# Kernel tuning notes

Hardware: AMD Instinct MI355X
Metric: run time of the kernel (lower is better)

Reference implementation:

```python
import jax, jax.numpy as jnp
import numpy as np

LAT = (4, 24, 24, 24, 24, 3, 3)  # [mu, L0, L1, L2, L3, 3, 3]


def setup_inputs() -> dict:
    key = jax.random.key(0)
    k1, k2 = jax.random.split(key)
    U_re = jax.random.normal(k1, LAT, dtype=jnp.float32)
    U_im = jax.random.normal(k2, LAT, dtype=jnp.float32)
    return {"U_re": U_re, "U_im": U_im}


def _polyakov_dir(Umu, axis, L):
    """P(x) = prod_{k=0}^{L-1} U_mu(x + k*mu_hat) via a sequential scan of
    batched 3x3 complex matmuls. Umu: [L0,L1,L2,L3,3,3] complex."""

    def step(carry, _):
        P, Ush = carry
        Ush = jnp.roll(Ush, -1, axis=axis)  # U_mu(x + (k)*mu_hat)
        P = jnp.einsum('...ij,...jk->...ik', P, Ush)
        return (P, Ush), None

    (P, _), _ = jax.lax.scan(step, (Umu, Umu), None, length=L - 1)
    return P


def reference(U_re, U_im):
    U = jax.lax.complex(U_re, U_im)  # complex64 link field
    loops = jnp.stack([
        _polyakov_dir(U[mu], mu, U.shape[1 + mu]) for mu in range(4)
    ])  # [4, L0, L1, L2, L3, 3, 3] complex
    # return real/imag stacked so output is a real array
    return jnp.stack([loops.real, loops.imag])
```

## Files before the change

kernel.cpp:

```cpp
#include <hip/hip_runtime.h>

#define LSIZE 24
#define VOL (LSIZE*LSIZE*LSIZE*LSIZE)
#define NLINES (LSIZE*LSIZE*LSIZE)
#define LPB 32
#define TPB 256
#define ESTRIDE 71
#define BUFW (18*ESTRIDE)

__device__ __forceinline__ void cmul(const float* __restrict__ ar, const float* __restrict__ ai,
                                     const float* __restrict__ br, const float* __restrict__ bi,
                                     float* __restrict__ or_, float* __restrict__ oi_) {
#pragma unroll
  for (int i = 0; i < 3; ++i) {
#pragma unroll
    for (int j = 0; j < 3; ++j) {
      float sr = 0.f, si = 0.f;
#pragma unroll
      for (int m = 0; m < 3; ++m) {
        float x = ar[i*3+m], y = ai[i*3+m];
        float u = br[m*3+j], v = bi[m*3+j];
        sr = fmaf(x, u, sr);
        sr = fmaf(-y, v, sr);
        si = fmaf(x, v, si);
        si = fmaf(y, u, si);
      }
      or_[i*3+j] = sr;
      oi_[i*3+j] = si;
    }
  }
}

__device__ __forceinline__ void cp9(float* dr, float* di, const float* sr, const float* si) {
#pragma unroll
  for (int e = 0; e < 9; ++e) { dr[e] = sr[e]; di[e] = si[e]; }
}

__device__ __forceinline__ void setid(float* r, float* im) {
#pragma unroll
  for (int e = 0; e < 9; ++e) { r[e] = (e == 0 || e == 4 || e == 8) ? 1.f : 0.f; im[e] = 0.f; }
}

__device__ __forceinline__ void shup(float* dr, float* di, const float* sr, const float* si, int delta) {
#pragma unroll
  for (int e = 0; e < 9; ++e) {
    dr[e] = __shfl_up(sr[e], (unsigned)delta, 64);
    di[e] = __shfl_up(si[e], (unsigned)delta, 64);
  }
}
__device__ __forceinline__ void shdn(float* dr, float* di, const float* sr, const float* si, int delta) {
#pragma unroll
  for (int e = 0; e < 9; ++e) {
    dr[e] = __shfl_down(sr[e], (unsigned)delta, 64);
    di[e] = __shfl_down(si[e], (unsigned)delta, 64);
  }
}

__global__ __launch_bounds__(TPB, 4) void polyakov_hyb(
    const float* __restrict__ U_re, const float* __restrict__ U_im,
    float* __restrict__ out) {
  __shared__ float buf[4 * BUFW];

  const int lane = threadIdx.x & 63;
  const int wv   = threadIdx.x >> 6;
  const int mu   = (blockIdx.x * LPB) / NLINES;

  int tl, ll, sh;
  if (mu == 3) { tl = lane & 7; ll = lane >> 3; sh = 1; }
  else         { tl = lane >> 3; ll = lane & 7; sh = 8; }

  const int l0 = blockIdx.x * LPB + wv * 8 - mu * NLINES;
  const int l  = l0 + ll;
  const int cC = l % LSIZE;
  const int cB = (l / LSIZE) % LSIZE;
  const int cA = l / (LSIZE*LSIZE);

  int x0, x1, x2, x3, st;
  if (mu == 0)      { x0 = 0;  x1 = cA; x2 = cB; x3 = cC; st = LSIZE*LSIZE*LSIZE; }
  else if (mu == 1) { x0 = cA; x1 = 0;  x2 = cB; x3 = cC; st = LSIZE*LSIZE; }
  else if (mu == 2) { x0 = cA; x1 = cB; x2 = 0;  x3 = cC; st = LSIZE; }
  else              { x0 = cA; x1 = cB; x2 = cC; x3 = 0;  st = 1; }
  const int s0 = ((x0*LSIZE + x1)*LSIZE + x2)*LSIZE + x3;
  const int k0 = 3 * tl;

  const float* __restrict__ gR = U_re + (size_t)mu * (VOL*9);
  const float* __restrict__ gI = U_im + (size_t)mu * (VOL*9);
  float* __restrict__ oR = out + (size_t)mu * (VOL*9);
  float* __restrict__ oI = out + (size_t)(4 + mu) * (VOL*9);

  auto ldU = [&](int kk, float* r, float* im_) {
    const float* p = gR + (size_t)(s0 + kk*st) * 9;
    const float* q = gI + (size_t)(s0 + kk*st) * 9;
#pragma unroll
    for (int e = 0; e < 9; ++e) { r[e] = p[e]; im_[e] = q[e]; }
  };

  float* wbuf = buf + wv * BUFW;

  auto emit = [&](const float* Vr, const float* Vi, int j) {
    if (mu == 3) {
      float* pr = oR + (size_t)(s0 + (k0 + j) * st) * 9;
      float* pi = oI + (size_t)(s0 + (k0 + j) * st) * 9;
#pragma unroll
      for (int e = 0; e < 9; ++e) { pr[e] = Vr[e]; pi[e] = Vi[e]; }
    } else {
      asm volatile("s_waitcnt lgkmcnt(0)" ::: "memory");
#pragma unroll
      for (int e = 0; e < 9; ++e) {
        wbuf[e * ESTRIDE + lane]       = Vr[e];
        wbuf[(9 + e) * ESTRIDE + lane] = Vi[e];
      }
      asm volatile("s_waitcnt lgkmcnt(0)" ::: "memory");
      __builtin_amdgcn_sched_barrier(0);
      const int s0w = s0 - ll;
      int slab = 0, rem = lane;
#pragma unroll
      for (int p = 0; p < 9; ++p) {
        int line8 = rem / 9;
        int e = rem - line8 * 9;
        int m = (slab << 3) + line8;
        float vr = wbuf[e * ESTRIDE + m];
        float vi = wbuf[(9 + e) * ESTRIDE + m];
        size_t off = (size_t)(s0w + (3 * slab + j) * st) * 9 + rem;
        oR[off] = vr;
        oI[off] = vi;
        int rem2 = rem + 64;
        int c = rem2 >= 72;
        rem = c ? rem2 - 72 : rem2;
        slab += c;
      }
    }
  };

  float Br[9], Bi[9];
  {
    float Ar[9], Ai[9], Cr[9], Ci[9], Tr0[9], Ti0[9];
    ldU(k0 + 0, Ar, Ai);
    ldU(k0 + 1, Cr, Ci);
    cmul(Ar, Ai, Cr, Ci, Tr0, Ti0);
    ldU(k0 + 2, Ar, Ai);
    cmul(Tr0, Ti0, Ar, Ai, Br, Bi);
  }

  float Yr[9], Yi[9], Tr[9], Ti[9];

  float Pr[9], Pi[9];
  {
    float Xr[9], Xi[9];
    cp9(Xr, Xi, Br, Bi);
#pragma unroll
    for (int d = 1; d < 8; d <<= 1) {
      shup(Yr, Yi, Xr, Xi, d * sh);
      if (tl >= d) { cmul(Yr, Yi, Xr, Xi, Tr, Ti); cp9(Xr, Xi, Tr, Ti); }
    }
    shup(Pr, Pi, Xr, Xi, sh);
    if (tl == 0) setid(Pr, Pi);
  }

  float Rr[9], Ri[9];
  {
    float Zr[9], Zi[9];
    cp9(Zr, Zi, Br, Bi);
#pragma unroll
    for (int d = 1; d < 8; d <<= 1) {
      shdn(Yr, Yi, Zr, Zi, d * sh);
      if (tl + d < 8) { cmul(Zr, Zi, Yr, Yi, Tr, Ti); cp9(Zr, Zi, Tr, Ti); }
    }
    shdn(Yr, Yi, Zr, Zi, sh);
    if (tl == 7) setid(Yr, Yi);
    cmul(Yr, Yi, Pr, Pi, Rr, Ri);
  }

  cmul(Br, Bi, Rr, Ri, Tr, Ti);
  emit(Tr, Ti, 0);

  float W2r[9], W2i[9], U1r[9], U1i[9];
  ldU(k0 + 2, Yr, Yi);
  cmul(Yr, Yi, Rr, Ri, W2r, W2i);
  ldU(k0 + 1, U1r, U1i);
  float W1r[9], W1i[9];
  cmul(U1r, U1i, W2r, W2i, W1r, W1i);
  ldU(k0 + 0, Pr, Pi);

  cmul(W1r, W1i, Pr, Pi, Tr, Ti);
  emit(Tr, Ti, 1);
  cmul(W2r, W2i, Pr, Pi, Yr, Yi);
  cmul(Yr, Yi, U1r, U1i, Tr, Ti);
  emit(Tr, Ti, 2);
}

extern "C" void kernel_launch(void* const* d_in, const int* in_sizes, int n_in,
                              void* d_out, int out_size, void* d_ws, size_t ws_size,
                              hipStream_t stream) {
  const float* U_re = (const float*)d_in[0];
  const float* U_im = (const float*)d_in[1];
  float* out = (float*)d_out;
  int nblocks = 4 * NLINES / LPB;
  hipLaunchKernelGGL(polyakov_hyb, dim3(nblocks), dim3(TPB), 0, stream, U_re, U_im, out);
}
```

Measured before the change: 212.6 us.

## Stage links through LDS with direct global-to-LDS loads and vectorized stores

```diff
diff --git a/kernel.cpp b/kernel.cpp
--- a/kernel.cpp
+++ b/kernel.cpp
@@ -3,10 +3,10 @@
 #define LSIZE 24
 #define VOL (LSIZE*LSIZE*LSIZE*LSIZE)
 #define NLINES (LSIZE*LSIZE*LSIZE)
-#define LPB 32
-#define TPB 256
-#define ESTRIDE 71
-#define BUFW (18*ESTRIDE)
+#define LPB 8
+#define TPB 64
+#define IMG 1728
+#define NCHUNK 864
 
 __device__ __forceinline__ void cmul(const float* __restrict__ ar, const float* __restrict__ ai,
                                      const float* __restrict__ br, const float* __restrict__ bi,
@@ -56,93 +56,75 @@
   }
 }
 
-__global__ __launch_bounds__(TPB, 4) void polyakov_hyb(
+__device__ __forceinline__ void ldm9(const float* __restrict__ L, float* v) {
+#pragma unroll
+  for (int e = 0; e < 9; ++e) v[e] = L[e];
+}
+__device__ __forceinline__ void stm9(float* __restrict__ L, const float* v) {
+#pragma unroll
+  for (int e = 0; e < 9; ++e) L[e] = v[e];
+}
+
+__global__ __launch_bounds__(TPB, 3) void polyakov_1w(
     const float* __restrict__ U_re, const float* __restrict__ U_im,
     float* __restrict__ out) {
-  __shared__ float buf[4 * BUFW];
+  __shared__ __align__(16) float lds[2 * IMG];
 
-  const int lane = threadIdx.x & 63;
-  const int wv   = threadIdx.x >> 6;
-  const int mu   = (blockIdx.x * LPB) / NLINES;
+  const int lane = threadIdx.x;
+  const int bid  = blockIdx.x;
+  const int mu   = bid / (NLINES / LPB);
+  const int l0   = (bid - mu * (NLINES / LPB)) * LPB;
 
-  int tl, ll, sh;
-  if (mu == 3) { tl = lane & 7; ll = lane >> 3; sh = 1; }
-  else         { tl = lane >> 3; ll = lane & 7; sh = 8; }
+  const int cC0 = l0 % LSIZE;
+  const int cB0 = (l0 / LSIZE) % LSIZE;
+  const int cA0 = l0 / (LSIZE * LSIZE);
 
-  const int l0 = blockIdx.x * LPB + wv * 8 - mu * NLINES;
-  const int l  = l0 + ll;
-  const int cC = l % LSIZE;
-  const int cB = (l / LSIZE) % LSIZE;
-  const int cA = l / (LSIZE*LSIZE);
-
-  int x0, x1, x2, x3, st;
-  if (mu == 0)      { x0 = 0;  x1 = cA; x2 = cB; x3 = cC; st = LSIZE*LSIZE*LSIZE; }
-  else if (mu == 1) { x0 = cA; x1 = 0;  x2 = cB; x3 = cC; st = LSIZE*LSIZE; }
-  else if (mu == 2) { x0 = cA; x1 = cB; x2 = 0;  x3 = cC; st = LSIZE; }
-  else              { x0 = cA; x1 = cB; x2 = cC; x3 = 0;  st = 1; }
-  const int s0 = ((x0*LSIZE + x1)*LSIZE + x2)*LSIZE + x3;
-  const int k0 = 3 * tl;
+  int s00, st;
+  if (mu == 0)      { s00 = l0;                                st = 13824; }
+  else if (mu == 1) { s00 = cA0*13824 + cB0*24  + cC0;         st = 576;   }
+  else if (mu == 2) { s00 = cA0*13824 + cB0*576 + cC0;         st = 24;    }
+  else              { s00 = l0 * 24;                           st = 1;     }
 
   const float* __restrict__ gR = U_re + (size_t)mu * (VOL*9);
   const float* __restrict__ gI = U_im + (size_t)mu * (VOL*9);
-  float* __restrict__ oR = out + (size_t)mu * (VOL*9);
-  float* __restrict__ oI = out + (size_t)(4 + mu) * (VOL*9);
 
-  auto ldU = [&](int kk, float* r, float* im_) {
-    const float* p = gR + (size_t)(s0 + kk*st) * 9;
-    const float* q = gI + (size_t)(s0 + kk*st) * 9;
 #pragma unroll
-    for (int e = 0; e < 9; ++e) { r[e] = p[e]; im_[e] = q[e]; }
-  };
+  for (int p = 0; p < 14; ++p) {
+    int c = p * 64 + lane;
+    if (c < NCHUNK) {
+      int d   = c << 2;
+      int arr = d >= IMG;
+      int da  = d - (arr ? IMG : 0);
+      int g;
+      if (mu == 3) g = s00 * 9 + da;
+      else { int slab = da / 72; g = (s00 + slab * st) * 9 + (da - slab * 72); }
+      const float* src = (arr ? gI : gR) + g;
+      __builtin_amdgcn_global_load_lds(
+          (const __attribute__((address_space(1))) void*)(const void*)src,
+          (__attribute__((address_space(3))) void*)(void*)(lds + p * 256),
+          16, 0, 0);
+    }
+  }
+  asm volatile("s_waitcnt vmcnt(0)" ::: "memory");
+  __builtin_amdgcn_sched_barrier(0);
 
-  float* wbuf = buf + wv * BUFW;
+  const int tl = lane >> 3;
+  const int ll = lane & 7;
+  const int k0 = 3 * tl;
+  const int uo = (mu == 3) ? ll * 216 : ll * 9;
+  const int ks = (mu == 3) ? 9 : 72;
+  float* mR = lds + uo;
+  float* mI = lds + IMG + uo;
 
-  auto emit = [&](const float* Vr, const float* Vi, int j) {
-    if (mu == 3) {
-      float* pr = oR + (size_t)(s0 + (k0 + j) * st) * 9;
-      float* pi = oI + (size_t)(s0 + (k0 + j) * st) * 9;
-#pragma unroll
-      for (int e = 0; e < 9; ++e) { pr[e] = Vr[e]; pi[e] = Vi[e]; }
-    } else {
-      asm volatile("s_waitcnt lgkmcnt(0)" ::: "memory");
-#pragma unroll
-      for (int e = 0; e < 9; ++e) {
-        wbuf[e * ESTRIDE + lane]       = Vr[e];
-        wbuf[(9 + e) * ESTRIDE + lane] = Vi[e];
-      }
-      asm volatile("s_waitcnt lgkmcnt(0)" ::: "memory");
-      __builtin_amdgcn_sched_barrier(0);
-      const int s0w = s0 - ll;
-      int slab = 0, rem = lane;
-#pragma unroll
-      for (int p = 0; p < 9; ++p) {
-        int line8 = rem / 9;
-        int e = rem - line8 * 9;
-        int m = (slab << 3) + line8;
-        float vr = wbuf[e * ESTRIDE + m];
-        float vi = wbuf[(9 + e) * ESTRIDE + m];
-        size_t off = (size_t)(s0w + (3 * slab + j) * st) * 9 + rem;
-        oR[off] = vr;
-        oI[off] = vi;
-        int rem2 = rem + 64;
-        int c = rem2 >= 72;
-        rem = c ? rem2 - 72 : rem2;
-        slab += c;
-      }
-    }
-  };
-
-  float Br[9], Bi[9];
+  float Br[9], Bi[9], Yr[9], Yi[9], Tr[9], Ti[9];
   {
-    float Ar[9], Ai[9], Cr[9], Ci[9], Tr0[9], Ti0[9];
-    ldU(k0 + 0, Ar, Ai);
-    ldU(k0 + 1, Cr, Ci);
-    cmul(Ar, Ai, Cr, Ci, Tr0, Ti0);
-    ldU(k0 + 2, Ar, Ai);
-    cmul(Tr0, Ti0, Ar, Ai, Br, Bi);
+    float Ar[9], Ai[9];
+    ldm9(mR + (k0+0)*ks, Yr); ldm9(mI + (k0+0)*ks, Yi);
+    ldm9(mR + (k0+1)*ks, Ar); ldm9(mI + (k0+1)*ks, Ai);
+    cmul(Yr, Yi, Ar, Ai, Tr, Ti);
+    ldm9(mR + (k0+2)*ks, Ar); ldm9(mI + (k0+2)*ks, Ai);
+    cmul(Tr, Ti, Ar, Ai, Br, Bi);
   }
-
-  float Yr[9], Yi[9], Tr[9], Ti[9];
 
   float Pr[9], Pi[9];
   {
@@ -150,43 +132,60 @@
     cp9(Xr, Xi, Br, Bi);
 #pragma unroll
     for (int d = 1; d < 8; d <<= 1) {
-      shup(Yr, Yi, Xr, Xi, d * sh);
+      shup(Yr, Yi, Xr, Xi, 8 * d);
       if (tl >= d) { cmul(Yr, Yi, Xr, Xi, Tr, Ti); cp9(Xr, Xi, Tr, Ti); }
     }
-    shup(Pr, Pi, Xr, Xi, sh);
+    shup(Pr, Pi, Xr, Xi, 8);
     if (tl == 0) setid(Pr, Pi);
   }
-
   float Rr[9], Ri[9];
   {
     float Zr[9], Zi[9];
     cp9(Zr, Zi, Br, Bi);
 #pragma unroll
     for (int d = 1; d < 8; d <<= 1) {
-      shdn(Yr, Yi, Zr, Zi, d * sh);
+      shdn(Yr, Yi, Zr, Zi, 8 * d);
       if (tl + d < 8) { cmul(Zr, Zi, Yr, Yi, Tr, Ti); cp9(Zr, Zi, Tr, Ti); }
     }
-    shdn(Yr, Yi, Zr, Zi, sh);
+    shdn(Yr, Yi, Zr, Zi, 8);
     if (tl == 7) setid(Yr, Yi);
     cmul(Yr, Yi, Pr, Pi, Rr, Ri);
   }
 
+  ldm9(mR + (k0+0)*ks, Pr); ldm9(mI + (k0+0)*ks, Pi);
   cmul(Br, Bi, Rr, Ri, Tr, Ti);
-  emit(Tr, Ti, 0);
+  stm9(mR + (k0+0)*ks, Tr); stm9(mI + (k0+0)*ks, Ti);
 
-  float W2r[9], W2i[9], U1r[9], U1i[9];
-  ldU(k0 + 2, Yr, Yi);
+  float W2r[9], W2i[9], U1r[9], U1i[9], W1r[9], W1i[9];
+  ldm9(mR + (k0+2)*ks, Yr); ldm9(mI + (k0+2)*ks, Yi);
   cmul(Yr, Yi, Rr, Ri, W2r, W2i);
-  ldU(k0 + 1, U1r, U1i);
-  float W1r[9], W1i[9];
+  ldm9(mR + (k0+1)*ks, U1r); ldm9(mI + (k0+1)*ks, U1i);
   cmul(U1r, U1i, W2r, W2i, W1r, W1i);
-  ldU(k0 + 0, Pr, Pi);
-
   cmul(W1r, W1i, Pr, Pi, Tr, Ti);
-  emit(Tr, Ti, 1);
+  stm9(mR + (k0+1)*ks, Tr); stm9(mI + (k0+1)*ks, Ti);
   cmul(W2r, W2i, Pr, Pi, Yr, Yi);
   cmul(Yr, Yi, U1r, U1i, Tr, Ti);
-  emit(Tr, Ti, 2);
+  stm9(mR + (k0+2)*ks, Tr); stm9(mI + (k0+2)*ks, Ti);
+
+  asm volatile("s_waitcnt lgkmcnt(0)" ::: "memory");
+  __builtin_amdgcn_sched_barrier(0);
+
+  float* __restrict__ oR = out + (size_t)mu * (VOL*9);
+  float* __restrict__ oI = out + (size_t)(4 + mu) * (VOL*9);
+#pragma unroll
+  for (int p = 0; p < 14; ++p) {
+    int c = p * 64 + lane;
+    if (c < NCHUNK) {
+      int d   = c << 2;
+      int arr = d >= IMG;
+      int da  = d - (arr ? IMG : 0);
+      int g;
+      if (mu == 3) g = s00 * 9 + da;
+      else { int slab = da / 72; g = (s00 + slab * st) * 9 + (da - slab * 72); }
+      float4 v = *(const float4*)(lds + d);
+      *(float4*)((arr ? oI : oR) + g) = v;
+    }
+  }
 }
 
 extern "C" void kernel_launch(void* const* d_in, const int* in_sizes, int n_in,
@@ -196,5 +195,5 @@
   const float* U_im = (const float*)d_in[1];
   float* out = (float*)d_out;
   int nblocks = 4 * NLINES / LPB;
-  hipLaunchKernelGGL(polyakov_hyb, dim3(nblocks), dim3(TPB), 0, stream, U_re, U_im, out);
+  hipLaunchKernelGGL(polyakov_1w, dim3(nblocks), dim3(TPB), 0, stream, U_re, U_im, out);
 }
```

Measured after the change: 178.5 us. -16.0%, faster.

## Vectorize LDS-staged output stores and drop reloads of link matrices

Applied to the files above, without the earlier changes.

```diff
diff --git a/kernel.cpp b/kernel.cpp
--- a/kernel.cpp
+++ b/kernel.cpp
@@ -3,10 +3,11 @@
 #define LSIZE 24
 #define VOL (LSIZE*LSIZE*LSIZE*LSIZE)
 #define NLINES (LSIZE*LSIZE*LSIZE)
-#define LPB 32
+#define LPW 8
+#define WPB 4
 #define TPB 256
-#define ESTRIDE 71
-#define BUFW (18*ESTRIDE)
+#define OCT (NLINES/LPW)
+#define OBUF 1152
 
 __device__ __forceinline__ void cmul(const float* __restrict__ ar, const float* __restrict__ ai,
                                      const float* __restrict__ br, const float* __restrict__ bi,
@@ -56,20 +57,21 @@
   }
 }
 
-__global__ __launch_bounds__(TPB, 4) void polyakov_hyb(
+__global__ __launch_bounds__(TPB, 4) void polyakov_js(
     const float* __restrict__ U_re, const float* __restrict__ U_im,
     float* __restrict__ out) {
-  __shared__ float buf[4 * BUFW];
+  __shared__ __align__(16) float obuf[WPB * OBUF];
 
   const int lane = threadIdx.x & 63;
   const int wv   = threadIdx.x >> 6;
-  const int mu   = (blockIdx.x * LPB) / NLINES;
+  const int O    = blockIdx.x * WPB + wv;
+  const int mu   = O / OCT;
+  const int l0   = (O - mu * OCT) * LPW;
 
   int tl, ll, sh;
   if (mu == 3) { tl = lane & 7; ll = lane >> 3; sh = 1; }
   else         { tl = lane >> 3; ll = lane & 7; sh = 8; }
 
-  const int l0 = blockIdx.x * LPB + wv * 8 - mu * NLINES;
   const int l  = l0 + ll;
   const int cC = l % LSIZE;
   const int cB = (l / LSIZE) % LSIZE;
@@ -95,52 +97,51 @@
     for (int e = 0; e < 9; ++e) { r[e] = p[e]; im_[e] = q[e]; }
   };
 
-  float* wbuf = buf + wv * BUFW;
+  float* wb = obuf + wv * OBUF;
 
   auto emit = [&](const float* Vr, const float* Vi, int j) {
     if (mu == 3) {
-      float* pr = oR + (size_t)(s0 + (k0 + j) * st) * 9;
-      float* pi = oI + (size_t)(s0 + (k0 + j) * st) * 9;
+      float* pr = oR + (size_t)(s0 + k0 + j) * 9;
+      float* pi = oI + (size_t)(s0 + k0 + j) * 9;
 #pragma unroll
       for (int e = 0; e < 9; ++e) { pr[e] = Vr[e]; pi[e] = Vi[e]; }
     } else {
       asm volatile("s_waitcnt lgkmcnt(0)" ::: "memory");
+      __builtin_amdgcn_sched_barrier(0);
+      const int wbase = tl * 72 + ll * 9;
 #pragma unroll
       for (int e = 0; e < 9; ++e) {
-        wbuf[e * ESTRIDE + lane]       = Vr[e];
-        wbuf[(9 + e) * ESTRIDE + lane] = Vi[e];
+        wb[wbase + e]       = Vr[e];
+        wb[576 + wbase + e] = Vi[e];
       }
       asm volatile("s_waitcnt lgkmcnt(0)" ::: "memory");
       __builtin_amdgcn_sched_barrier(0);
-      const int s0w = s0 - ll;
-      int slab = 0, rem = lane;
+      const int s00x9 = (s0 - ll) * 9;
 #pragma unroll
-      for (int p = 0; p < 9; ++p) {
-        int line8 = rem / 9;
-        int e = rem - line8 * 9;
-        int m = (slab << 3) + line8;
-        float vr = wbuf[e * ESTRIDE + m];
-        float vi = wbuf[(9 + e) * ESTRIDE + m];
-        size_t off = (size_t)(s0w + (3 * slab + j) * st) * 9 + rem;
-        oR[off] = vr;
-        oI[off] = vi;
-        int rem2 = rem + 64;
-        int c = rem2 >= 72;
-        rem = c ? rem2 - 72 : rem2;
-        slab += c;
+      for (int p = 0; p < 5; ++p) {
+        int c = p * 64 + lane;
+        if (c < 288) {
+          int arr  = c >= 144;
+          int ca   = c - (arr ? 144 : 0);
+          int slab = ca / 18;
+          int rem  = ca - slab * 18;
+          float4 v = *(const float4*)(wb + arr * 576 + slab * 72 + rem * 4);
+          float* g = (arr ? oI : oR) + (size_t)(s00x9 + (3 * slab + j) * st * 9 + rem * 4);
+          *(float4*)g = v;
+        }
       }
     }
   };
 
-  float Br[9], Bi[9];
-  {
-    float Ar[9], Ai[9], Cr[9], Ci[9], Tr0[9], Ti0[9];
-    ldU(k0 + 0, Ar, Ai);
-    ldU(k0 + 1, Cr, Ci);
-    cmul(Ar, Ai, Cr, Ci, Tr0, Ti0);
-    ldU(k0 + 2, Ar, Ai);
-    cmul(Tr0, Ti0, Ar, Ai, Br, Bi);
-  }
+  float U0r[9], U0i[9], U1r[9], U1i[9], U2r[9], U2i[9];
+  ldU(k0 + 0, U0r, U0i);
+  ldU(k0 + 1, U1r, U1i);
+  ldU(k0 + 2, U2r, U2i);
+
+  float A1r[9], A1i[9], Br[9], Bi[9], S1r[9], S1i[9];
+  cmul(U0r, U0i, U1r, U1i, A1r, A1i);
+  cmul(A1r, A1i, U2r, U2i, Br,  Bi);
+  cmul(U1r, U1i, U2r, U2i, S1r, S1i);
 
   float Yr[9], Yi[9], Tr[9], Ti[9];
 
@@ -156,7 +157,6 @@
     shup(Pr, Pi, Xr, Xi, sh);
     if (tl == 0) setid(Pr, Pi);
   }
-
   float Rr[9], Ri[9];
   {
     float Zr[9], Zi[9];
@@ -174,18 +174,12 @@
   cmul(Br, Bi, Rr, Ri, Tr, Ti);
   emit(Tr, Ti, 0);
 
-  float W2r[9], W2i[9], U1r[9], U1i[9];
-  ldU(k0 + 2, Yr, Yi);
-  cmul(Yr, Yi, Rr, Ri, W2r, W2i);
-  ldU(k0 + 1, U1r, U1i);
-  float W1r[9], W1i[9];
-  cmul(U1r, U1i, W2r, W2i, W1r, W1i);
-  ldU(k0 + 0, Pr, Pi);
+  cmul(Rr, Ri, U0r, U0i, Yr, Yi);
+  cmul(S1r, S1i, Yr, Yi, Tr, Ti);
+  emit(Tr, Ti, 1);
 
-  cmul(W1r, W1i, Pr, Pi, Tr, Ti);
-  emit(Tr, Ti, 1);
-  cmul(W2r, W2i, Pr, Pi, Yr, Yi);
-  cmul(Yr, Yi, U1r, U1i, Tr, Ti);
+  cmul(Rr, Ri, A1r, A1i, Yr, Yi);
+  cmul(U2r, U2i, Yr, Yi, Tr, Ti);
   emit(Tr, Ti, 2);
 }
 
@@ -195,6 +189,6 @@
   const float* U_re = (const float*)d_in[0];
   const float* U_im = (const float*)d_in[1];
   float* out = (float*)d_out;
-  int nblocks = 4 * NLINES / LPB;
-  hipLaunchKernelGGL(polyakov_hyb, dim3(nblocks), dim3(TPB), 0, stream, U_re, U_im, out);
+  int nblocks = 4 * OCT / WPB;
+  hipLaunchKernelGGL(polyakov_js, dim3(nblocks), dim3(TPB), 0, stream, U_re, U_im, out);
 }
```

After: 247.3 us. +16.4%, slower.
